# Optimization experiments

Measured on AMD Instinct MI355X. Metric: run time of the kernel, lower is better.

Reference implementation:

```python
import jax, jax.numpy as jnp
import numpy as np

KS = 21        # kernel_size
SIGMA = 5.0    # sigma
C = 3          # channels
PAD = KS // 2  # reflection pad = 10


def _gaussian_kernel():
    # Matches torch construction: 2D isotropic Gaussian on integer grid, then
    # normalized to sum 1. Separable => outer product of 1D Gaussians.
    coords = jnp.arange(KS, dtype=jnp.float32)
    mean = (KS - 1) / 2.0
    g1 = jnp.exp(-((coords - mean) ** 2) / (2.0 * SIGMA ** 2))
    k2 = jnp.outer(g1, g1)
    k2 = k2 / jnp.sum(k2)
    # depthwise weight [C, 1, KS, KS] (OIHW with feature_group_count=C)
    return jnp.tile(k2[None, None, :, :], (C, 1, 1, 1))


def setup_inputs() -> dict:
    key = jax.random.key(0)
    x = jax.random.normal(key, (32, 3, 512, 512), dtype=jnp.float32)
    return {"x": x}


def reference(x):
    w = _gaussian_kernel()
    xp = jnp.pad(x, ((0, 0), (0, 0), (PAD, PAD), (PAD, PAD)), mode="reflect")
    out = jax.lax.conv_general_dilated(
        xp, w,
        window_strides=(1, 1),
        padding="VALID",
        dimension_numbers=("NCHW", "OIHW", "NCHW"),
        feature_group_count=C,
    )
    return out  # [B, C, H, W], same spatial size as input
```

## Files before the change

### kernel.cpp

```cpp
#include <hip/hip_runtime.h>
#include <math.h>


#define KS    21
#define PAD   10
#define TILE  64
#define LW    (TILE + 2 * PAD)
#define SKEW  2
#define LWX   92
#define SH    64
#define IMG_H 512
#define IMG_W 512
#define NT    256

__global__ __launch_bounds__(NT) void gauss_blur_kernel(
    const float* __restrict__ in, float* __restrict__ out)
{
    __shared__ __align__(16) float s_in[LW * LWX];
    __shared__ __align__(16) float s_h [LW * SH];

    float w[KS];
    {
        float s = 0.f;
#pragma unroll
        for (int k = 0; k < KS; ++k) {
            float d = (float)(k - PAD);
            w[k] = expf(-d * d * (1.0f / 50.0f));
            s += w[k];
        }
        float inv = 1.0f / s;
#pragma unroll
        for (int k = 0; k < KS; ++k) w[k] *= inv;
    }

    const int tid   = threadIdx.x;
    const int plane = blockIdx.z;
    const int x0    = blockIdx.x * TILE;
    const int y0    = blockIdx.y * TILE;
    const int xbase = x0 - PAD - SKEW;

    const float* __restrict__ pin = in + (size_t)plane * (IMG_H * IMG_W);

    if (xbase >= 0 && xbase + LWX <= IMG_W) {
        for (int idx = tid; idx < LW * (LWX / 4); idx += NT) {
            int ly = idx / (LWX / 4);
            int q  = idx - ly * (LWX / 4);
            int gy = y0 + ly - PAD;
            gy = (gy < 0) ? -gy : ((gy >= IMG_H) ? (2 * IMG_H - 2 - gy) : gy);
            float4 v = *(const float4*)&pin[gy * IMG_W + xbase + 4 * q];
            *(float4*)&s_in[ly * LWX + 4 * q] = v;
        }
    } else {
        for (int idx = tid; idx < LW * LWX; idx += NT) {
            int ly = idx / LWX;
            int j  = idx - ly * LWX;
            int gy = y0 + ly - PAD;
            int gx = xbase + j;
            gy = (gy < 0) ? -gy : ((gy >= IMG_H) ? (2 * IMG_H - 2 - gy) : gy);
            gx = (gx < 0) ? -gx : ((gx >= IMG_W) ? (2 * IMG_W - 2 - gx) : gx);
            s_in[idx] = pin[gy * IMG_W + gx];
        }
    }
    __syncthreads();

    for (int idx = tid; idx < LW * (TILE / 4); idx += NT) {
        int ly = idx >> 4;
        int lx = (idx & 15) << 2;
        const float4* rp = (const float4*)&s_in[ly * LWX + lx];
        float v[28];
#pragma unroll
        for (int t = 0; t < 7; ++t) {
            float4 f = rp[t];
            v[4 * t + 0] = f.x; v[4 * t + 1] = f.y;
            v[4 * t + 2] = f.z; v[4 * t + 3] = f.w;
        }
        float a0 = 0.f, a1 = 0.f, a2 = 0.f, a3 = 0.f;
#pragma unroll
        for (int k = 0; k < KS; ++k) {
            float wk = w[k];
            a0 += wk * v[k + 2];
            a1 += wk * v[k + 3];
            a2 += wk * v[k + 4];
            a3 += wk * v[k + 5];
        }
        *(float4*)&s_h[ly * SH + lx] = make_float4(a0, a1, a2, a3);
    }
    __syncthreads();

    {
        const int c  = tid & 63;
        const int rb = (tid >> 6) << 4;

        float acc[16];
#pragma unroll
        for (int r = 0; r < 16; ++r) acc[r] = 0.f;

#pragma unroll
        for (int t = 0; t < KS + 15; ++t) {
            float v = s_h[(rb + t) * SH + c];
#pragma unroll
            for (int r = 0; r < 16; ++r) {
                int k = t - r;
                if (k >= 0 && k < KS) acc[r] += w[k] * v;
            }
        }

        float* __restrict__ pout = out + (size_t)plane * (IMG_H * IMG_W)
                                       + (size_t)(y0 + rb) * IMG_W + (x0 + c);
#pragma unroll
        for (int r = 0; r < 16; ++r) pout[r * IMG_W] = acc[r];
    }
}

extern "C" void kernel_launch(void* const* d_in, const int* in_sizes, int n_in,
                              void* d_out, int out_size, void* d_ws, size_t ws_size,
                              hipStream_t stream)
{
    const float* x = (const float*)d_in[0];
    float* out = (float*)d_out;

    dim3 grid(IMG_W / TILE, IMG_H / TILE, 96);
    dim3 block(NT);
    gauss_blur_kernel<<<grid, block, 0, stream>>>(x, out);
}
```

Measured before the change: 228.7 us.

## Compute horizontal pass in place in input LDS, drop second shared buffer

Removes the separate horizontal-result shared buffer and writes the horizontal pass results back into the input tile in place. Each thread now handles a 16-wide output strip per row, loading 40 values into registers before any write, with a sched_barrier so all reads complete before the overwrite. Launch bounds now request 5 blocks per CU. The goal is less LDS per block and therefore higher occupancy, at the cost of more register pressure and fewer, larger work items in the horizontal pass.

```diff
diff --git a/kernel.cpp b/kernel.cpp
--- a/kernel.cpp
+++ b/kernel.cpp
@@ -8,16 +8,14 @@
 #define LW    (TILE + 2 * PAD)
 #define SKEW  2
 #define LWX   92
-#define SH    64
 #define IMG_H 512
 #define IMG_W 512
 #define NT    256
 
-__global__ __launch_bounds__(NT) void gauss_blur_kernel(
+__global__ __launch_bounds__(NT, 5) void gauss_blur_kernel(
     const float* __restrict__ in, float* __restrict__ out)
 {
     __shared__ __align__(16) float s_in[LW * LWX];
-    __shared__ __align__(16) float s_h [LW * SH];
 
     float w[KS];
     {
@@ -63,27 +61,37 @@
     }
     __syncthreads();
 
-    for (int idx = tid; idx < LW * (TILE / 4); idx += NT) {
-        int ly = idx >> 4;
-        int lx = (idx & 15) << 2;
-        const float4* rp = (const float4*)&s_in[ly * LWX + lx];
-        float v[28];
 #pragma unroll
-        for (int t = 0; t < 7; ++t) {
-            float4 f = rp[t];
-            v[4 * t + 0] = f.x; v[4 * t + 1] = f.y;
-            v[4 * t + 2] = f.z; v[4 * t + 3] = f.w;
+    for (int it = 0; it < 2; ++it) {
+        int idx = tid + it * NT;
+        if (idx < LW * 4) {
+            int y  = idx >> 2;
+            int cb = (idx & 3) << 4;
+            const float4* rp = (const float4*)&s_in[y * LWX + cb];
+            float v[40];
+#pragma unroll
+            for (int t = 0; t < 10; ++t) {
+                float4 f = rp[t];
+                v[4 * t + 0] = f.x; v[4 * t + 1] = f.y;
+                v[4 * t + 2] = f.z; v[4 * t + 3] = f.w;
+            }
+            __builtin_amdgcn_sched_barrier(0);
+            float* wp = &s_in[y * LWX + cb];
+#pragma unroll
+            for (int ob = 0; ob < 4; ++ob) {
+                float a0 = 0.f, a1 = 0.f, a2 = 0.f, a3 = 0.f;
+#pragma unroll
+                for (int k = 0; k < KS; ++k) {
+                    float wk = w[k];
+                    int b = 4 * ob + 2 + k;
+                    a0 += wk * v[b + 0];
+                    a1 += wk * v[b + 1];
+                    a2 += wk * v[b + 2];
+                    a3 += wk * v[b + 3];
+                }
+                *(float4*)(wp + 4 * ob) = make_float4(a0, a1, a2, a3);
+            }
         }
-        float a0 = 0.f, a1 = 0.f, a2 = 0.f, a3 = 0.f;
-#pragma unroll
-        for (int k = 0; k < KS; ++k) {
-            float wk = w[k];
-            a0 += wk * v[k + 2];
-            a1 += wk * v[k + 3];
-            a2 += wk * v[k + 4];
-            a3 += wk * v[k + 5];
-        }
-        *(float4*)&s_h[ly * SH + lx] = make_float4(a0, a1, a2, a3);
     }
     __syncthreads();
 
@@ -97,7 +105,7 @@
 
 #pragma unroll
         for (int t = 0; t < KS + 15; ++t) {
-            float v = s_h[(rb + t) * SH + c];
+            float v = s_in[(rb + t) * LWX + c];
 #pragma unroll
             for (int r = 0; r < 16; ++r) {
                 int k = t - r;
```

Result: faster. 201.0 us (-12.1%).
